# Optimization experiments

Measured on AMD Instinct MI355X. Metric: run time of the kernel, lower is better.

## Reference

```python
import jax, jax.numpy as jnp
import numpy as np

N, E, F = 32768, 524288, 16          # nodes, edges, num_filters
S_IN, V_IN = 64, 32                  # input irreps: 64x0e + 32x1o  (dim 64 + 96 = 160)
NRBF = 32                            # radial basis size of f_ij
LN2 = float(np.log(2.0))

def ssp(x):
    # shifted softplus, the standard SchNet activation
    return jax.nn.softplus(x) - LN2

def setup_inputs() -> dict:
    key = jax.random.key(0)
    ks = jax.random.split(key, 16)
    x = jax.random.normal(ks[0], (N, S_IN + 3 * V_IN), jnp.float32)
    idx_i = jax.random.randint(ks[1], (E,), 0, N)
    idx_j = jax.random.randint(ks[2], (E,), 0, N)
    f_ij = jax.random.normal(ks[3], (E, NRBF), jnp.float32)
    rcut_ij = jax.random.uniform(ks[4], (E,), jnp.float32)
    Yr_ij = jax.random.normal(ks[5], (E, 4), jnp.float32)  # 1x0e + 1x1o
    # equivariant Linear 1: (64x0e+32x1o) -> num_filters*(1x0e+1x1o) = 16x0e+16x1o
    W1_0e = jax.random.normal(ks[6], (S_IN, F), jnp.float32)
    W1_1o = jax.random.normal(ks[7], (V_IN, F), jnp.float32)
    # filter MLP: NRBF -> F -> num_irreps(6*F)
    mW1 = jax.random.normal(ks[8], (NRBF, F), jnp.float32) / np.sqrt(NRBF)
    mb1 = jnp.zeros((F,), jnp.float32)
    mW2 = jax.random.normal(ks[9], (F, 6 * F), jnp.float32) / np.sqrt(F)
    mb2 = jnp.zeros((6 * F,), jnp.float32)
    # equivariant Linear 2: (2Fx0e+2Fx1o+Fx1e+Fx2e) -> input irreps (1e/2e paths drop)
    W2_0e = jax.random.normal(ks[10], (2 * F, S_IN), jnp.float32)
    W2_1o = jax.random.normal(ks[11], (2 * F, V_IN), jnp.float32)
    # equivariant Linear 3: input irreps -> input irreps
    W3_0e = jax.random.normal(ks[12], (S_IN, S_IN), jnp.float32)
    W3_1o = jax.random.normal(ks[13], (V_IN, V_IN), jnp.float32)
    return dict(x=x, f_ij=f_ij, rcut_ij=rcut_ij, Yr_ij=Yr_ij,
                W1_0e=W1_0e, W1_1o=W1_1o, mW1=mW1, mb1=mb1, mW2=mW2, mb2=mb2,
                W2_0e=W2_0e, W2_1o=W2_1o, W3_0e=W3_0e, W3_1o=W3_1o,
                idx_i=idx_i, idx_j=idx_j)

def reference(x, f_ij, rcut_ij, Yr_ij, W1_0e, W1_1o, mW1, mb1, mW2, mb2,
              W2_0e, W2_1o, W3_0e, W3_1o, idx_i, idx_j):
    n = x.shape[0]
    s = x[:, :S_IN]                                  # [N, 64]  0e channels
    v = x[:, S_IN:].reshape(n, V_IN, 3)              # [N, 32, 3] 1o channels
    # Linear 1 (per-irrep channel mixing, e3nn fan-in normalization)
    s1 = (s @ W1_0e) / np.sqrt(S_IN)                 # [N, F]
    v1 = jnp.einsum('ncd,cf->nfd', v, W1_1o) / np.sqrt(V_IN)  # [N, F, 3]
    # gather neighbor features (x_j = x[idx_j], mul_to_axis -> per-filter irreps)
    sj = s1[idx_j]                                   # [E, F]
    vj = v1[idx_j]                                   # [E, F, 3]
    y0 = Yr_ij[:, 0]                                 # [E]
    y1 = Yr_ij[:, 1:4]                               # [E, 3]
    # tensor product (0e+1o) x (0e+1o) -> 2x0e + 2x1o + 1x1e + 1x2e, per filter
    o0a = sj * y0[:, None]                                            # 0e: 0e x 0e
    o0b = jnp.einsum('efd,ed->ef', vj, y1) / np.sqrt(3.0)             # 0e: 1o.1o
    o1a = sj[:, :, None] * y1[:, None, :]                             # 1o: 0e x 1o
    o1b = vj * y0[:, None, None]                                      # 1o: 1o x 0e
    o1e = jnp.cross(vj, y1[:, None, :]) / np.sqrt(2.0)                # 1e: 1o ^ 1o
    ux, uy, uz = vj[..., 0], vj[..., 1], vj[..., 2]
    wx, wy, wz = y1[:, None, 0], y1[:, None, 1], y1[:, None, 2]
    o2 = jnp.stack([(ux * wy + uy * wx) / np.sqrt(2.0),
                    (uy * wz + uz * wy) / np.sqrt(2.0),
                    (2.0 * uz * wz - ux * wx - uy * wy) / np.sqrt(6.0),
                    (ux * wz + uz * wx) / np.sqrt(2.0),
                    (ux * wx - uy * wy) / np.sqrt(2.0)], axis=-1)      # 2e [E, F, 5]
    # filter MLP on radial features, gated by cutoff; one scalar per irrep
    W = ssp(f_ij @ mW1 + mb1) @ mW2 + mb2            # [E, 6F]
    W = W * rcut_ij[:, None]
    w0a, w0b, w1a, w1b, w1e, w2 = (W[:, k * F:(k + 1) * F] for k in range(6))
    seg = lambda z: jax.ops.segment_sum(z, idx_i, num_segments=N)
    # modulate + scatter-sum into center atoms
    n0a = seg(o0a * w0a); n0b = seg(o0b * w0b)                          # [N, F]
    n1a = seg(o1a * w1a[:, :, None]); n1b = seg(o1b * w1b[:, :, None])  # [N, F, 3]
    n1e = seg(o1e * w1e[:, :, None])                                    # [N, F, 3] (dropped by Linear 2)
    n2 = seg(o2 * w2[:, :, None])                                       # [N, F, 5] (dropped by Linear 2)
    n0 = jnp.concatenate([n0a, n0b], axis=-1)        # [N, 2F] 0e
    n1 = jnp.concatenate([n1a, n1b], axis=1)         # [N, 2F, 3] 1o
    del n1e, n2  # no matching output irrep in input_irreps -> e3nn Linear drops them
    # Linear 2 back to input irreps
    s2 = (n0 @ W2_0e) / np.sqrt(2 * F)               # [N, 64]
    v2 = jnp.einsum('nfd,fc->ncd', n1, W2_1o) / np.sqrt(2 * F)  # [N, 32, 3]
    # scalar activation on l=0 only
    s2 = ssp(s2)
    # Linear 3
    s3 = (s2 @ W3_0e) / np.sqrt(S_IN)
    v3 = jnp.einsum('ncd,ce->ned', v2, W3_1o) / np.sqrt(V_IN)
    return jnp.concatenate([s3, v3.reshape(n, -1)], axis=-1)  # [N, 160]
```

## Files before the change

### kernel.cpp

```cpp
#include <hip/hip_runtime.h>
#include <math.h>

#define NN 32768
#define NE 524288

__device__ __forceinline__ float sspf(float x) {
    float r = fmaxf(x, 0.0f) + log1pf(expf(-fabsf(x)));
    return r - 0.69314718055994530942f;
}

__global__ __launch_bounds__(256) void hist_kernel(
    const int* __restrict__ idx_i, int* __restrict__ counts)
{
    int e = blockIdx.x * 256 + threadIdx.x;
    atomicAdd(&counts[idx_i[e]], 1);
}

__global__ __launch_bounds__(1024) void scan_kernel(
    const int* __restrict__ counts, int* __restrict__ start, int* __restrict__ cursor)
{
    __shared__ int tmp[1024];
    int tid = threadIdx.x;
    int base = tid * 32;
    int local[32];
    int sum = 0;
    const int4* c4 = (const int4*)(counts + base);
#pragma unroll
    for (int q = 0; q < 8; q++) {
        int4 v = c4[q];
        local[q*4+0] = sum; sum += v.x;
        local[q*4+1] = sum; sum += v.y;
        local[q*4+2] = sum; sum += v.z;
        local[q*4+3] = sum; sum += v.w;
    }
    tmp[tid] = sum;
    __syncthreads();
    for (int off = 1; off < 1024; off <<= 1) {
        int v = 0;
        if (tid >= off) v = tmp[tid - off];
        __syncthreads();
        if (tid >= off) tmp[tid] += v;
        __syncthreads();
    }
    int excl = tmp[tid] - sum;
#pragma unroll
    for (int k = 0; k < 32; k++) {
        int s = excl + local[k];
        start[base + k] = s;
        cursor[base + k] = s;
    }
    if (tid == 1023) start[NN] = tmp[1023];
}

__global__ __launch_bounds__(256) void pack_kernel(
    const float* __restrict__ f_ij,
    const float* __restrict__ rcut_ij,
    const float* __restrict__ Yr,
    const int*   __restrict__ idx_i,
    const int*   __restrict__ idx_j,
    const float* __restrict__ mW1,
    const float* __restrict__ mb1,
    int* __restrict__ cursor,
    float* __restrict__ epack)
{
    __shared__ float sW1[512];
    __shared__ float sb1[16];
    int t = threadIdx.x;
    for (int k = t; k < 512; k += 256) sW1[k] = mW1[k];
    if (t < 16) sb1[t] = mb1[t];
    __syncthreads();

    int e = blockIdx.x * 256 + t;
    float h[16];
#pragma unroll
    for (int f = 0; f < 16; f++) h[f] = sb1[f];
    const float4* frow = (const float4*)(f_ij + (size_t)e * 32);
#pragma unroll
    for (int rq = 0; rq < 8; rq++) {
        float4 fv = frow[rq];
        int r = rq * 4;
#pragma unroll
        for (int f = 0; f < 16; f++)
            h[f] += fv.x * sW1[(r+0)*16+f] + fv.y * sW1[(r+1)*16+f]
                  + fv.z * sW1[(r+2)*16+f] + fv.w * sW1[(r+3)*16+f];
    }
    float rc = rcut_ij[e];
#pragma unroll
    for (int f = 0; f < 16; f++) h[f] = sspf(h[f]) * rc;

    int i = idx_i[e];
    int j = idx_j[e];
    float4 y = ((const float4*)Yr)[e];
    int slot = atomicAdd(&cursor[i], 1);

    float* rec = epack + (size_t)slot * 24;
    float4* r4 = (float4*)rec;
#pragma unroll
    for (int q = 0; q < 4; q++) r4[q] = ((float4*)h)[q];
    r4[4] = y;
    rec[20] = rc;
    rec[21] = __int_as_float(j);
    rec[22] = 0.f;
    rec[23] = 0.f;
}

__global__ __launch_bounds__(256) void embed_kernel(
    const float* __restrict__ x,
    const float* __restrict__ W1s,
    const float* __restrict__ W1v,
    float* __restrict__ embed)
{
    __shared__ float sWs[1024];
    __shared__ float sWv[512];
    int t = threadIdx.x;
    for (int k = t; k < 1024; k += 256) sWs[k] = W1s[k];
    for (int k = t; k < 512;  k += 256) sWv[k] = W1v[k];
    __syncthreads();

    int n = blockIdx.x * 256 + t;
    const float* xr = x + (size_t)n * 160;

    float s1[16];
#pragma unroll
    for (int f = 0; f < 16; f++) s1[f] = 0.f;
#pragma unroll
    for (int cq = 0; cq < 16; cq++) {
        float4 sv = ((const float4*)xr)[cq];
        int c = cq * 4;
#pragma unroll
        for (int f = 0; f < 16; f++) {
            s1[f] += sv.x * sWs[(c+0)*16+f] + sv.y * sWs[(c+1)*16+f]
                   + sv.z * sWs[(c+2)*16+f] + sv.w * sWs[(c+3)*16+f];
        }
    }

    float v1[48];
#pragma unroll
    for (int k = 0; k < 48; k++) v1[k] = 0.f;
#pragma unroll
    for (int q = 0; q < 24; q++) {
        float4 vv = ((const float4*)(xr + 64))[q];
        float vals[4] = {vv.x, vv.y, vv.z, vv.w};
#pragma unroll
        for (int u = 0; u < 4; u++) {
            int m = q * 4 + u;
            int c = m / 3, d = m % 3;
            float val = vals[u];
#pragma unroll
            for (int f = 0; f < 16; f++)
                v1[f*3+d] += val * sWv[c*16+f];
        }
    }

    float ob[64];
    const float is32 = 0.17677669529663688f;
#pragma unroll
    for (int f = 0; f < 16; f++) {
        ob[f]      = s1[f] * 0.125f;
        ob[16 + f] = v1[f*3+0] * is32;
        ob[32 + f] = v1[f*3+1] * is32;
        ob[48 + f] = v1[f*3+2] * is32;
    }

    float4* eo = (float4*)(embed + (size_t)n * 64);
#pragma unroll
    for (int q = 0; q < 16; q++) eo[q] = ((float4*)ob)[q];
}

__global__ __launch_bounds__(256) void nodeagg_kernel(
    const float* __restrict__ embed,
    const float* __restrict__ epack,
    const int*   __restrict__ start,
    const float* __restrict__ mW2,
    const float* __restrict__ mb2,
    float* __restrict__ acc)
{
    __shared__ float sW2[1024];
    int t = threadIdx.x;
    for (int k = t; k < 1024; k += 256)
        sW2[k] = mW2[(k >> 6) * 96 + (k & 63)];
    __syncthreads();

    int gid = blockIdx.x * 256 + t;
    int node = gid >> 4;
    int f = gid & 15;

    float wga[16], wgb[16], wgc[16], wgd[16];
#pragma unroll
    for (int k = 0; k < 16; k++) {
        wga[k] = sW2[k*64 + f];
        wgb[k] = sW2[k*64 + 16 + f];
        wgc[k] = sW2[k*64 + 32 + f];
        wgd[k] = sW2[k*64 + 48 + f];
    }
    float b0a = mb2[f], b0b = mb2[16+f], b1a = mb2[32+f], b1b = mb2[48+f];

    float aa = 0.f, ab = 0.f;
    float A1a0 = 0.f, A1a1 = 0.f, A1a2 = 0.f;
    float A1b0 = 0.f, A1b1 = 0.f, A1b2 = 0.f;

    int s0 = start[node];
    int s1 = start[node+1];

    for (int q = s0; q < s1; q++) {
        const float* rec = epack + (size_t)q * 24;
        const float4* r4 = (const float4*)rec;
        float4 h0 = r4[0], h1 = r4[1], h2 = r4[2], h3 = r4[3];
        float4 y  = r4[4];
        float rc  = rec[20];
        int j = __float_as_int(rec[21]);

        const float* em = embed + (size_t)j * 64;
        float sj = em[f];
        float vx = em[16 + f];
        float vy = em[32 + f];
        float vz = em[48 + f];

        float w0a = rc*b0a, w0b = rc*b0b, w1a = rc*b1a, w1b = rc*b1b;
        float h[16] = {h0.x,h0.y,h0.z,h0.w, h1.x,h1.y,h1.z,h1.w,
                       h2.x,h2.y,h2.z,h2.w, h3.x,h3.y,h3.z,h3.w};
#pragma unroll
        for (int k = 0; k < 16; k++) {
            w0a += h[k] * wga[k];
            w0b += h[k] * wgb[k];
            w1a += h[k] * wgc[k];
            w1b += h[k] * wgd[k];
        }

        aa += sj * y.x * w0a;
        ab += (vx*y.y + vy*y.z + vz*y.w) * w0b;
        float sw = sj * w1a;
        A1a0 += sw * y.y;
        A1a1 += sw * y.z;
        A1a2 += sw * y.w;
        float yw = y.x * w1b;
        A1b0 += vx * yw;
        A1b1 += vy * yw;
        A1b2 += vz * yw;
    }

    const float is3 = 0.5773502691896258f;
    float* o = acc + (size_t)node * 128;
    o[f]       = aa;
    o[16 + f]  = ab * is3;
    o[32 + f]  = A1a0;
    o[48 + f]  = A1a1;
    o[64 + f]  = A1a2;
    o[80 + f]  = A1b0;
    o[96 + f]  = A1b1;
    o[112 + f] = A1b2;
}

__global__ __launch_bounds__(256) void out_kernel(
    const float* __restrict__ acc,
    const float* __restrict__ W2s,
    const float* __restrict__ W2v,
    const float* __restrict__ W3s,
    const float* __restrict__ W3v,
    float* __restrict__ out)
{
    __shared__ float sW2s[2048];
    __shared__ float sW2v[1024];
    __shared__ float sW3s[4096];
    __shared__ float sW3v[1024];
    __shared__ float Lbuf[4][288];
    int t = threadIdx.x;
    for (int k = t; k < 2048; k += 256) sW2s[k] = W2s[k];
    for (int k = t; k < 1024; k += 256) sW2v[k] = W2v[k];
    for (int k = t; k < 4096; k += 256) sW3s[k] = W3s[k];
    for (int k = t; k < 1024; k += 256) sW3v[k] = W3v[k];
    __syncthreads();

    int wv = t >> 6, ln = t & 63;
    float* L = Lbuf[wv];
    const float is32 = 0.17677669529663688f;

    int c1 = ln / 3, d1 = ln % 3;
    int o2i = 64 + ln;
    int c2 = o2i / 3, d2 = o2i % 3;

    for (int it = 0; it < 16; it++) {
        int n = blockIdx.x * 64 + it * 4 + wv;
        const float* a = acc + (size_t)n * 128;
        float2 av = ((const float2*)a)[ln];
        ((float2*)L)[ln] = av;
        __syncthreads();

        float s_acc = 0.f;
#pragma unroll
        for (int g = 0; g < 32; g++) s_acc += L[g] * sW2s[g*64 + ln];
        float s2 = sspf(s_acc * is32);

        float v2a = 0.f, v2b = 0.f;
        int ba1 = 32 + d1*16, bb1 = 80 + d1*16;
        int ba2 = 32 + d2*16, bb2 = 80 + d2*16;
#pragma unroll
        for (int f = 0; f < 16; f++) {
            v2a += L[ba1+f] * sW2v[f*32 + c1];
            v2a += L[bb1+f] * sW2v[(16+f)*32 + c1];
            if (ln < 32) {
                v2b += L[ba2+f] * sW2v[f*32 + c2];
                v2b += L[bb2+f] * sW2v[(16+f)*32 + c2];
            }
        }

        L[128 + ln] = s2;
        L[192 + ln] = v2a * is32;
        if (ln < 32) L[192 + 64 + ln] = v2b * is32;
        __syncthreads();

        float s3 = 0.f;
#pragma unroll
        for (int k = 0; k < 64; k++) s3 += L[128+k] * sW3s[k*64 + ln];
        out[(size_t)n*160 + ln] = s3 * 0.125f;

        float a1 = 0.f;
#pragma unroll
        for (int c = 0; c < 32; c++) a1 += L[192 + c*3 + d1] * sW3v[c*32 + c1];
        out[(size_t)n*160 + 64 + ln] = a1 * is32;
        if (ln < 32) {
            float a2 = 0.f;
#pragma unroll
            for (int c = 0; c < 32; c++) a2 += L[192 + c*3 + d2] * sW3v[c*32 + c2];
            out[(size_t)n*160 + 64 + o2i] = a2 * is32;
        }
        __syncthreads();
    }
}

extern "C" void kernel_launch(void* const* d_in, const int* in_sizes, int n_in,
                              void* d_out, int out_size, void* d_ws, size_t ws_size,
                              hipStream_t stream) {
    const float* x     = (const float*)d_in[0];
    const float* f_ij  = (const float*)d_in[1];
    const float* rcut  = (const float*)d_in[2];
    const float* Yr    = (const float*)d_in[3];
    const float* W1s   = (const float*)d_in[4];
    const float* W1v   = (const float*)d_in[5];
    const float* mW1   = (const float*)d_in[6];
    const float* mb1   = (const float*)d_in[7];
    const float* mW2   = (const float*)d_in[8];
    const float* mb2   = (const float*)d_in[9];
    const float* W2s   = (const float*)d_in[10];
    const float* W2v   = (const float*)d_in[11];
    const float* W3s   = (const float*)d_in[12];
    const float* W3v   = (const float*)d_in[13];
    const int*   idx_i = (const int*)d_in[14];
    const int*   idx_j = (const int*)d_in[15];
    float* out = (float*)d_out;

    float* fws   = (float*)d_ws;
    float* embed = fws;
    float* acc   = embed + (size_t)NN * 64;
    float* epack = acc   + (size_t)NN * 128;
    int* ibase   = (int*)(epack + (size_t)NE * 24);
    int* counts  = ibase;
    int* start   = counts + NN;
    int* cursor  = start + NN + 1;

    hipMemsetAsync(counts, 0, (size_t)NN * sizeof(int), stream);
    hist_kernel<<<NE/256, 256, 0, stream>>>(idx_i, counts);
    scan_kernel<<<1, 1024, 0, stream>>>(counts, start, cursor);
    pack_kernel<<<NE/256, 256, 0, stream>>>(f_ij, rcut, Yr, idx_i, idx_j,
                                            mW1, mb1, cursor, epack);
    embed_kernel<<<NN/256, 256, 0, stream>>>(x, W1s, W1v, embed);
    nodeagg_kernel<<<(NN*16)/256, 256, 0, stream>>>(embed, epack, start, mW2, mb2, acc);
    out_kernel<<<512, 256, 0, stream>>>(acc, W2s, W2v, W3s, W3v, out);
}
```

Before: 375.5 us.

## Restructure output kernel to one thread per node with register-tiled matvecs

Replaces the wave-per-node output kernel, which staged weights and activations in LDS behind block barriers, with a thread-per-node design. Half the block computes the scalar path and the other half the vector path. Weights are read directly from global memory as wave-uniform loads, and outputs are written with float4 stores. This removes the LDS traffic and barriers, but uses many registers and does strided, uncoalesced per-thread row loads and stores, so occupancy and memory efficiency may drop.

Result: slower. 423.2 us (+12.7%).

```diff
diff --git a/kernel.cpp b/kernel.cpp
--- a/kernel.cpp
+++ b/kernel.cpp
@@ -259,72 +259,104 @@
     const float* __restrict__ W3v,
     float* __restrict__ out)
 {
-    __shared__ float sW2s[2048];
-    __shared__ float sW2v[1024];
-    __shared__ float sW3s[4096];
-    __shared__ float sW3v[1024];
-    __shared__ float Lbuf[4][288];
     int t = threadIdx.x;
-    for (int k = t; k < 2048; k += 256) sW2s[k] = W2s[k];
-    for (int k = t; k < 1024; k += 256) sW2v[k] = W2v[k];
-    for (int k = t; k < 4096; k += 256) sW3s[k] = W3s[k];
-    for (int k = t; k < 1024; k += 256) sW3v[k] = W3v[k];
-    __syncthreads();
-
-    int wv = t >> 6, ln = t & 63;
-    float* L = Lbuf[wv];
+    int role = t >> 7;
+    int n = blockIdx.x * 128 + (t & 127);
+    const float* a = acc + (size_t)n * 128;
+    float* o = out + (size_t)n * 160;
     const float is32 = 0.17677669529663688f;
 
-    int c1 = ln / 3, d1 = ln % 3;
-    int o2i = 64 + ln;
-    int c2 = o2i / 3, d2 = o2i % 3;
-
-    for (int it = 0; it < 16; it++) {
-        int n = blockIdx.x * 64 + it * 4 + wv;
-        const float* a = acc + (size_t)n * 128;
-        float2 av = ((const float2*)a)[ln];
-        ((float2*)L)[ln] = av;
-        __syncthreads();
-
-        float s_acc = 0.f;
-#pragma unroll
-        for (int g = 0; g < 32; g++) s_acc += L[g] * sW2s[g*64 + ln];
-        float s2 = sspf(s_acc * is32);
-
-        float v2a = 0.f, v2b = 0.f;
-        int ba1 = 32 + d1*16, bb1 = 80 + d1*16;
-        int ba2 = 32 + d2*16, bb2 = 80 + d2*16;
-#pragma unroll
-        for (int f = 0; f < 16; f++) {
-            v2a += L[ba1+f] * sW2v[f*32 + c1];
-            v2a += L[bb1+f] * sW2v[(16+f)*32 + c1];
-            if (ln < 32) {
-                v2b += L[ba2+f] * sW2v[f*32 + c2];
-                v2b += L[bb2+f] * sW2v[(16+f)*32 + c2];
+    if (role == 0) {
+        float n0[32];
+#pragma unroll
+        for (int q = 0; q < 8; q++) ((float4*)n0)[q] = ((const float4*)a)[q];
+
+        float s2[64];
+#pragma unroll
+        for (int c0 = 0; c0 < 64; c0 += 16) {
+            float t16[16];
+#pragma unroll
+            for (int u = 0; u < 16; u++) t16[u] = 0.f;
+#pragma unroll
+            for (int k = 0; k < 32; k++) {
+                float nk = n0[k];
+#pragma unroll
+                for (int u = 0; u < 16; u++)
+                    t16[u] += nk * W2s[k*64 + c0 + u];
             }
-        }
-
-        L[128 + ln] = s2;
-        L[192 + ln] = v2a * is32;
-        if (ln < 32) L[192 + 64 + ln] = v2b * is32;
-        __syncthreads();
-
-        float s3 = 0.f;
-#pragma unroll
-        for (int k = 0; k < 64; k++) s3 += L[128+k] * sW3s[k*64 + ln];
-        out[(size_t)n*160 + ln] = s3 * 0.125f;
-
-        float a1 = 0.f;
-#pragma unroll
-        for (int c = 0; c < 32; c++) a1 += L[192 + c*3 + d1] * sW3v[c*32 + c1];
-        out[(size_t)n*160 + 64 + ln] = a1 * is32;
-        if (ln < 32) {
-            float a2 = 0.f;
-#pragma unroll
-            for (int c = 0; c < 32; c++) a2 += L[192 + c*3 + d2] * sW3v[c*32 + c2];
-            out[(size_t)n*160 + 64 + o2i] = a2 * is32;
-        }
-        __syncthreads();
+#pragma unroll
+            for (int u = 0; u < 16; u++) s2[c0+u] = sspf(t16[u] * is32);
+        }
+
+#pragma unroll
+        for (int c0 = 0; c0 < 64; c0 += 16) {
+            float t16[16];
+#pragma unroll
+            for (int u = 0; u < 16; u++) t16[u] = 0.f;
+#pragma unroll
+            for (int k = 0; k < 64; k++) {
+                float sk = s2[k];
+#pragma unroll
+                for (int u = 0; u < 16; u++)
+                    t16[u] += sk * W3s[k*64 + c0 + u];
+            }
+            float4 r0 = {t16[0]*0.125f,  t16[1]*0.125f,  t16[2]*0.125f,  t16[3]*0.125f};
+            float4 r1 = {t16[4]*0.125f,  t16[5]*0.125f,  t16[6]*0.125f,  t16[7]*0.125f};
+            float4 r2 = {t16[8]*0.125f,  t16[9]*0.125f,  t16[10]*0.125f, t16[11]*0.125f};
+            float4 r3 = {t16[12]*0.125f, t16[13]*0.125f, t16[14]*0.125f, t16[15]*0.125f};
+            ((float4*)(o + c0))[0] = r0;
+            ((float4*)(o + c0))[1] = r1;
+            ((float4*)(o + c0))[2] = r2;
+            ((float4*)(o + c0))[3] = r3;
+        }
+    } else {
+        float v3buf[96];
+#pragma unroll
+        for (int d = 0; d < 3; d++) {
+            float na[16], nb[16];
+            const float4* pa = (const float4*)(a + 32 + 16*d);
+            const float4* pb = (const float4*)(a + 80 + 16*d);
+#pragma unroll
+            for (int q = 0; q < 4; q++) { ((float4*)na)[q] = pa[q]; ((float4*)nb)[q] = pb[q]; }
+
+            float v2[32];
+#pragma unroll
+            for (int c0 = 0; c0 < 32; c0 += 16) {
+                float t16[16];
+#pragma unroll
+                for (int u = 0; u < 16; u++) t16[u] = 0.f;
+#pragma unroll
+                for (int f = 0; f < 16; f++) {
+                    float fa = na[f], fbv = nb[f];
+#pragma unroll
+                    for (int u = 0; u < 16; u++) {
+                        t16[u] += fa  * W2v[f*32 + c0 + u];
+                        t16[u] += fbv * W2v[(16+f)*32 + c0 + u];
+                    }
+                }
+#pragma unroll
+                for (int u = 0; u < 16; u++) v2[c0+u] = t16[u] * is32;
+            }
+
+#pragma unroll
+            for (int e0 = 0; e0 < 32; e0 += 16) {
+                float t16[16];
+#pragma unroll
+                for (int u = 0; u < 16; u++) t16[u] = 0.f;
+#pragma unroll
+                for (int c = 0; c < 32; c++) {
+                    float vc = v2[c];
+#pragma unroll
+                    for (int u = 0; u < 16; u++)
+                        t16[u] += vc * W3v[c*32 + e0 + u];
+                }
+#pragma unroll
+                for (int u = 0; u < 16; u++) v3buf[(e0+u)*3 + d] = t16[u] * is32;
+            }
+        }
+        float4* ov = (float4*)(o + 64);
+#pragma unroll
+        for (int q = 0; q < 24; q++) ov[q] = ((float4*)v3buf)[q];
     }
 }
 
@@ -365,5 +397,5 @@
                                             mW1, mb1, cursor, epack);
     embed_kernel<<<NN/256, 256, 0, stream>>>(x, W1s, W1v, embed);
     nodeagg_kernel<<<(NN*16)/256, 256, 0, stream>>>(embed, epack, start, mW2, mb2, acc);
-    out_kernel<<<512, 256, 0, stream>>>(acc, W2s, W2v, W3s, W3v, out);
-}
+    out_kernel<<<NN/128, 256, 0, stream>>>(acc, W2s, W2v, W3s, W3v, out);
+}
```
